# Performance work log

Hardware: AMD Instinct MI355X
Metric: run time of the kernel (lower is better)

## Reference

```python
import jax, jax.numpy as jnp
import numpy as np

N = 100000   # nodes
E = 1600000  # edges
D = 128      # in_dim
H = 128      # hidden_dim
G = 128      # graphs in batch


def setup_inputs() -> dict:
    key = jax.random.key(0)
    ks = jax.random.split(key, 16)
    inp = {
        "x": jax.random.normal(ks[0], (N, D), dtype=jnp.float32),
        "edge_index": jax.random.randint(ks[1], (2, E), 0, N, dtype=jnp.int32),
        "batch": jnp.sort(jax.random.randint(ks[2], (N,), 0, G, dtype=jnp.int32)),
    }
    dims = [(D, H), (H, H), (H, H)]
    k = 3
    for i, (di, dh) in enumerate(dims):
        inp[f"W1_{i}"] = jax.random.normal(ks[k], (di, dh), jnp.float32) * 0.05; k += 1
        inp[f"b1_{i}"] = jnp.zeros((dh,), jnp.float32)
        inp[f"W2_{i}"] = jax.random.normal(ks[k], (dh, dh), jnp.float32) * 0.05; k += 1
        inp[f"b2_{i}"] = jnp.zeros((dh,), jnp.float32)
    return inp


def _gin_layer(x, edge_index, W1, b1, W2, b2):
    # GINConv, eps=0: h_i = MLP(x_i + sum_{j->i} x_j)
    src, dst = edge_index[0], edge_index[1]
    agg = jax.ops.segment_sum(x[src], dst, num_segments=N)  # [N, d]
    h = x + agg
    h = jnp.maximum(h @ W1 + b1, 0.0)  # dropout = identity (eval)
    return h @ W2 + b2


def reference(x, edge_index, batch,
              W1_0, b1_0, W2_0, b2_0,
              W1_1, b1_1, W2_1, b2_1,
              W1_2, b1_2, W2_2, b2_2):
    params = [(W1_0, b1_0, W2_0, b2_0),
              (W1_1, b1_1, W2_1, b2_1),
              (W1_2, b1_2, W2_2, b2_2)]
    h = x
    for (W1, b1, W2, b2) in params:
        h = _gin_layer(h, edge_index, W1, b1, W2, b2)
    # global_mean_pool over batch indices
    sums = jax.ops.segment_sum(h, batch, num_segments=G)             # [G, H]
    cnts = jax.ops.segment_sum(jnp.ones((N,), h.dtype), batch, num_segments=G)
    return sums / jnp.maximum(cnts, 1.0)[:, None]
```

## Files before the change

### kernel.cpp

```cpp
#include <hip/hip_runtime.h>
#include <stdint.h>

#define NN 100000
#define NE 1600000
#define DD 128
#define NG 128
#define NPX 12500
#define NBS 25

using f32x4  = __attribute__((ext_vector_type(4))) float;
using bf16x8 = __attribute__((ext_vector_type(8))) __bf16;

__device__ __forceinline__ unsigned short f2bf(float f) {
  unsigned int u = __builtin_bit_cast(unsigned int, f);
  u = (u + 0x7FFFu + ((u >> 16) & 1u)) >> 16;
  return (unsigned short)u;
}

__device__ __forceinline__ float2 bfu(unsigned int u) {
  float2 r;
  r.x = __builtin_bit_cast(float, u << 16);
  r.y = __builtin_bit_cast(float, u & 0xffff0000u);
  return r;
}

__device__ __forceinline__ void addu4(float* a, uint4 v) {
  float2 p0 = bfu(v.x), p1 = bfu(v.y), p2 = bfu(v.z), p3 = bfu(v.w);
  a[0] += p0.x; a[1] += p0.y; a[2] += p1.x; a[3] += p1.y;
  a[4] += p2.x; a[5] += p2.y; a[6] += p3.x; a[7] += p3.y;
}

union ABu { uint4 q; bf16x8 v; };

__global__ void k_count(const int* __restrict__ dst, int* __restrict__ deg) {
  int xcd = blockIdx.x & 7;
  int e = (blockIdx.x >> 3) * 256 + threadIdx.x;
  if (e >= NE) return;
  int d = dst[e];
  if ((unsigned)(d - xcd * NPX) < (unsigned)NPX) atomicAdd(&deg[d], 1);
}

__global__ __launch_bounds__(1024) void k_scanA(const int* __restrict__ deg,
                                                int* __restrict__ rowptr,
                                                int* __restrict__ bsum) {
  __shared__ int wsum[16];
  const int tid = threadIdx.x, wid = tid >> 6, lane = tid & 63;
  int idx = blockIdx.x * 4096 + tid * 4;
  int v0 = (idx + 0 < NN) ? deg[idx + 0] : 0;
  int v1 = (idx + 1 < NN) ? deg[idx + 1] : 0;
  int v2 = (idx + 2 < NN) ? deg[idx + 2] : 0;
  int v3 = (idx + 3 < NN) ? deg[idx + 3] : 0;
  int tsum = v0 + v1 + v2 + v3;
  int sc = tsum;
  #pragma unroll
  for (int off = 1; off < 64; off <<= 1) {
    int n = __shfl_up(sc, off);
    if (lane >= off) sc += n;
  }
  if (lane == 63) wsum[wid] = sc;
  __syncthreads();
  if (wid == 0 && lane < 16) {
    int w = wsum[lane];
    #pragma unroll
    for (int off = 1; off < 16; off <<= 1) {
      int n = __shfl_up(w, off);
      if (lane >= off) w += n;
    }
    wsum[lane] = w;
  }
  __syncthreads();
  int excl = (wid ? wsum[wid - 1] : 0) + sc - tsum;
  if (idx     <= NN) rowptr[idx]     = excl;
  if (idx + 1 <= NN) rowptr[idx + 1] = excl + v0;
  if (idx + 2 <= NN) rowptr[idx + 2] = excl + v0 + v1;
  if (idx + 3 <= NN) rowptr[idx + 3] = excl + v0 + v1 + v2;
  if (tid == 1023) bsum[blockIdx.x] = wsum[15];
}

__global__ void k_scanB(int* __restrict__ bsum) {
  int lane = threadIdx.x & 63;
  int v = (lane < NBS) ? bsum[lane] : 0;
  int sc = v;
  #pragma unroll
  for (int off = 1; off < 64; off <<= 1) {
    int n = __shfl_up(sc, off);
    if (lane >= off) sc += n;
  }
  if (lane < NBS) bsum[lane] = sc - v;
}

__global__ __launch_bounds__(1024) void k_scanC(int* __restrict__ rowptr,
                                                const int* __restrict__ bsum) {
  int add = bsum[blockIdx.x];
  int idx = blockIdx.x * 4096 + threadIdx.x * 4;
  if (idx     <= NN) rowptr[idx]     += add;
  if (idx + 1 <= NN) rowptr[idx + 1] += add;
  if (idx + 2 <= NN) rowptr[idx + 2] += add;
  if (idx + 3 <= NN) rowptr[idx + 3] += add;
}

__global__ void k_fill(const int* __restrict__ src, const int* __restrict__ dst,
                       const int* __restrict__ rowptr, int* __restrict__ cursor,
                       int* __restrict__ csr) {
  int xcd = blockIdx.x & 7;
  int e = (blockIdx.x >> 3) * 256 + threadIdx.x;
  if (e >= NE) return;
  int d = dst[e];
  if ((unsigned)(d - xcd * NPX) < (unsigned)NPX) {
    int pos = rowptr[d] + atomicAdd(&cursor[d], 1);
    csr[pos] = src[e];
  }
}

__global__ void k_wconv(const float* __restrict__ w0, const float* __restrict__ w1,
                        const float* __restrict__ w2, const float* __restrict__ w3,
                        const float* __restrict__ w4, const float* __restrict__ w5,
                        unsigned short* __restrict__ wt) {
  int idx = blockIdx.x * 256 + threadIdx.x;
  if (idx >= 6 * 16384) return;
  int m = idx >> 14, rem = idx & 16383;
  int n = rem >> 7, k = rem & 127;
  const float* W = (m == 0) ? w0 : (m == 1) ? w1 : (m == 2) ? w2
                 : (m == 3) ? w3 : (m == 4) ? w4 : w5;
  wt[idx] = f2bf(W[k * 128 + n]);
}

__global__ void k_xconv(const float* __restrict__ x, unsigned short* __restrict__ xb) {
  int i = blockIdx.x * 256 + threadIdx.x;
  if (i >= NN * DD / 4) return;
  float4 v = ((const float4*)x)[i];
  uint2 p;
  p.x = (unsigned int)f2bf(v.x) | ((unsigned int)f2bf(v.y) << 16);
  p.y = (unsigned int)f2bf(v.z) | ((unsigned int)f2bf(v.w) << 16);
  ((uint2*)xb)[i] = p;
}

__global__ __launch_bounds__(64) void k_gin(const unsigned short* __restrict__ hb,
                                            const int* __restrict__ rowptr,
                                            const int* __restrict__ csr,
                                            const unsigned short* __restrict__ w1t,
                                            const float* __restrict__ b1,
                                            const unsigned short* __restrict__ w2t,
                                            const float* __restrict__ b2,
                                            unsigned short* __restrict__ hout) {
  __shared__ unsigned short wt_[16 * DD];
  const int lane = threadIdx.x;
  const int r16  = lane & 15;
  const int kg   = lane >> 4;
  const int waveBase = blockIdx.x * 16;
  const uint4* h4 = (const uint4*)hb;

  #pragma unroll
  for (int it = 0; it < 4; ++it) {
    const int lrow = it * 4 + kg;
    const int node = waveBase + lrow;
    float acc[8] = {0.f,0.f,0.f,0.f,0.f,0.f,0.f,0.f};
    if (node < NN) {
      addu4(acc, h4[(size_t)node * 16 + r16]);
      int j = rowptr[node];
      const int je = rowptr[node + 1];
      for (; j + 7 < je; j += 8) {
        int s0 = csr[j],     s1 = csr[j + 1], s2 = csr[j + 2], s3 = csr[j + 3];
        int s4 = csr[j + 4], s5 = csr[j + 5], s6 = csr[j + 6], s7 = csr[j + 7];
        uint4 v0 = h4[(size_t)s0 * 16 + r16];
        uint4 v1 = h4[(size_t)s1 * 16 + r16];
        uint4 v2 = h4[(size_t)s2 * 16 + r16];
        uint4 v3 = h4[(size_t)s3 * 16 + r16];
        uint4 v4 = h4[(size_t)s4 * 16 + r16];
        uint4 v5 = h4[(size_t)s5 * 16 + r16];
        uint4 v6 = h4[(size_t)s6 * 16 + r16];
        uint4 v7 = h4[(size_t)s7 * 16 + r16];
        addu4(acc, v0); addu4(acc, v1); addu4(acc, v2); addu4(acc, v3);
        addu4(acc, v4); addu4(acc, v5); addu4(acc, v6); addu4(acc, v7);
      }
      for (; j + 3 < je; j += 4) {
        int s0 = csr[j], s1 = csr[j + 1], s2 = csr[j + 2], s3 = csr[j + 3];
        uint4 v0 = h4[(size_t)s0 * 16 + r16];
        uint4 v1 = h4[(size_t)s1 * 16 + r16];
        uint4 v2 = h4[(size_t)s2 * 16 + r16];
        uint4 v3 = h4[(size_t)s3 * 16 + r16];
        addu4(acc, v0); addu4(acc, v1); addu4(acc, v2); addu4(acc, v3);
      }
      for (; j < je; ++j) addu4(acc, h4[(size_t)csr[j] * 16 + r16]);
    }
    uint4 p;
    p.x = (unsigned int)f2bf(acc[0]) | ((unsigned int)f2bf(acc[1]) << 16);
    p.y = (unsigned int)f2bf(acc[2]) | ((unsigned int)f2bf(acc[3]) << 16);
    p.z = (unsigned int)f2bf(acc[4]) | ((unsigned int)f2bf(acc[5]) << 16);
    p.w = (unsigned int)f2bf(acc[6]) | ((unsigned int)f2bf(acc[7]) << 16);
    *(uint4*)(wt_ + lrow * DD + ((r16 ^ (lrow & 7)) << 3)) = p;
  }

  f32x4 acc[8];
  #pragma unroll
  for (int nb = 0; nb < 8; ++nb) acc[nb] = (f32x4){0.f, 0.f, 0.f, 0.f};
  #pragma unroll
  for (int s = 0; s < 4; ++s) {
    ABu au;
    au.q = *(const uint4*)(wt_ + r16 * DD + ((((s << 2) + kg) ^ (r16 & 7)) << 3));
    #pragma unroll
    for (int nb = 0; nb < 8; ++nb) {
      ABu bu; bu.q = *(const uint4*)(w1t + (nb * 16 + r16) * DD + s * 32 + kg * 8);
      acc[nb] = __builtin_amdgcn_mfma_f32_16x16x32_bf16(au.v, bu.v, acc[nb], 0, 0, 0);
    }
  }
  #pragma unroll
  for (int nb = 0; nb < 8; ++nb) {
    int n = nb * 16 + r16;
    float bias = b1[n];
    #pragma unroll
    for (int reg = 0; reg < 4; ++reg) {
      int urow = (kg << 2) + reg;
      float v = acc[nb][reg] + bias;
      v = v > 0.f ? v : 0.f;
      wt_[urow * DD + ((((n >> 3) ^ (urow & 7)) << 3) | (n & 7))] = f2bf(v);
    }
  }

  #pragma unroll
  for (int nb = 0; nb < 8; ++nb) acc[nb] = (f32x4){0.f, 0.f, 0.f, 0.f};
  #pragma unroll
  for (int s = 0; s < 4; ++s) {
    ABu au;
    au.q = *(const uint4*)(wt_ + r16 * DD + ((((s << 2) + kg) ^ (r16 & 7)) << 3));
    #pragma unroll
    for (int nb = 0; nb < 8; ++nb) {
      ABu bu; bu.q = *(const uint4*)(w2t + (nb * 16 + r16) * DD + s * 32 + kg * 8);
      acc[nb] = __builtin_amdgcn_mfma_f32_16x16x32_bf16(au.v, bu.v, acc[nb], 0, 0, 0);
    }
  }
  #pragma unroll
  for (int reg = 0; reg < 4; ++reg) {
    int row = waveBase + (kg << 2) + reg;
    if (row < NN) {
      #pragma unroll
      for (int nb = 0; nb < 8; ++nb) {
        int n = nb * 16 + r16;
        hout[row * DD + n] = f2bf(acc[nb][reg] + b2[n]);
      }
    }
  }
}

__global__ __launch_bounds__(256) void k_pool(const unsigned short* __restrict__ hb,
                                              const int* __restrict__ batch,
                                              float* __restrict__ out) {
  const int g  = blockIdx.x;
  const int f2 = threadIdx.x & 63;
  const int rp = threadIdx.x >> 6;
  int lo = 0, hi = NN;
  while (lo < hi) { int m = (lo + hi) >> 1; if (batch[m] < g) lo = m + 1; else hi = m; }
  const int start = lo;
  hi = NN;
  while (lo < hi) { int m = (lo + hi) >> 1; if (batch[m] < g + 1) lo = m + 1; else hi = m; }
  const int end = lo;

  const unsigned int* h32 = (const unsigned int*)hb;
  float2 acc = {0.f, 0.f};
  int i = start + rp;
  for (; i + 4 < end; i += 8) {
    float2 a = bfu(h32[(size_t)i * 64 + f2]);
    float2 b = bfu(h32[(size_t)(i + 4) * 64 + f2]);
    acc.x += a.x + b.x; acc.y += a.y + b.y;
  }
  for (; i < end; i += 4) {
    float2 a = bfu(h32[(size_t)i * 64 + f2]);
    acc.x += a.x; acc.y += a.y;
  }

  __shared__ float2 part[4][64];
  part[rp][f2] = acc;
  __syncthreads();
  if (rp == 0) {
    float2 t0 = part[0][f2], t1 = part[1][f2], t2 = part[2][f2], t3 = part[3][f2];
    float inv = 1.0f / (float)max(end - start, 1);
    out[g * DD + 2 * f2]     = (t0.x + t1.x + t2.x + t3.x) * inv;
    out[g * DD + 2 * f2 + 1] = (t0.y + t1.y + t2.y + t3.y) * inv;
  }
}

extern "C" void kernel_launch(void* const* d_in, const int* in_sizes, int n_in,
                              void* d_out, int out_size, void* d_ws, size_t ws_size,
                              hipStream_t stream) {
  const float* x    = (const float*)d_in[0];
  const int* ei     = (const int*)d_in[1];
  const int* src    = ei;
  const int* dst    = ei + NE;
  const int* batch  = (const int*)d_in[2];

  char* ws = (char*)d_ws;
  size_t off = 0;
  auto alloc = [&](size_t bytes) { char* p = ws + off; off = (off + bytes + 255) & ~(size_t)255; return p; };

  int*  deg    = (int*)alloc(2 * NN * 4);
  int*  cursor = deg + NN;
  int*  rowptr = (int*)alloc((NN + 1) * 4);
  int*  bsum   = (int*)alloc(NBS * 4);
  int*  csr    = (int*)alloc(NE * 4);
  unsigned short* wt = (unsigned short*)alloc(6 * 16384 * 2);
  unsigned short* xb = (unsigned short*)alloc((size_t)NN * DD * 2);
  unsigned short* hA = (unsigned short*)alloc((size_t)NN * DD * 2);
  unsigned short* hB = (unsigned short*)alloc((size_t)NN * DD * 2);

  hipMemsetAsync(deg, 0, 2 * NN * 4, stream);

  k_wconv<<<(6 * 16384 + 255) / 256, 256, 0, stream>>>(
      (const float*)d_in[3], (const float*)d_in[5],
      (const float*)d_in[7], (const float*)d_in[9],
      (const float*)d_in[11], (const float*)d_in[13], wt);
  k_xconv<<<(NN * DD / 4 + 255) / 256, 256, 0, stream>>>(x, xb);

  const int echunks = (NE + 255) / 256;
  k_count<<<8 * echunks, 256, 0, stream>>>(dst, deg);
  k_scanA<<<NBS, 1024, 0, stream>>>(deg, rowptr, bsum);
  k_scanB<<<1, 64, 0, stream>>>(bsum);
  k_scanC<<<NBS, 1024, 0, stream>>>(rowptr, bsum);
  k_fill<<<8 * echunks, 256, 0, stream>>>(src, dst, rowptr, cursor, csr);

  const unsigned short* hin = xb;
  unsigned short* houts[3] = {hA, hB, hA};
  for (int l = 0; l < 3; ++l) {
    k_gin<<<(NN + 15) / 16, 64, 0, stream>>>(
        hin, rowptr, csr,
        wt + (2 * l) * 16384, (const float*)d_in[4 + 4 * l],
        wt + (2 * l + 1) * 16384, (const float*)d_in[6 + 4 * l], houts[l]);
    hin = houts[l];
  }

  k_pool<<<NG, 256, 0, stream>>>(hin, batch, (float*)d_out);
}
```

Baseline: 612.5 us.

## Split GIN block work across four waves for gather and MLP

Each 16-node block now runs on four waves instead of one. Each wave gathers neighbour sums for 4 nodes, and in the two MLP GEMMs each wave computes 2 of the 8 output column tiles. Barriers are added between the gather, the first GEMM, the ReLU writeback to shared memory, and the second GEMM. The aim is more memory-level parallelism in the latency-bound gather and less serial work per wave, at the cost of block-wide synchronisation and more threads per block.

Result: faster. 589.0 us (-3.8%).

```diff
diff --git a/kernel.cpp b/kernel.cpp
--- a/kernel.cpp
+++ b/kernel.cpp
@@ -135,25 +135,25 @@
   ((uint2*)xb)[i] = p;
 }
 
-__global__ __launch_bounds__(64) void k_gin(const unsigned short* __restrict__ hb,
-                                            const int* __restrict__ rowptr,
-                                            const int* __restrict__ csr,
-                                            const unsigned short* __restrict__ w1t,
-                                            const float* __restrict__ b1,
-                                            const unsigned short* __restrict__ w2t,
-                                            const float* __restrict__ b2,
-                                            unsigned short* __restrict__ hout) {
+__global__ __launch_bounds__(256) void k_gin(const unsigned short* __restrict__ hb,
+                                             const int* __restrict__ rowptr,
+                                             const int* __restrict__ csr,
+                                             const unsigned short* __restrict__ w1t,
+                                             const float* __restrict__ b1,
+                                             const unsigned short* __restrict__ w2t,
+                                             const float* __restrict__ b2,
+                                             unsigned short* __restrict__ hout) {
   __shared__ unsigned short wt_[16 * DD];
-  const int lane = threadIdx.x;
+  const int wv   = threadIdx.x >> 6;
+  const int lane = threadIdx.x & 63;
   const int r16  = lane & 15;
   const int kg   = lane >> 4;
-  const int waveBase = blockIdx.x * 16;
+  const int blockBase = blockIdx.x * 16;
   const uint4* h4 = (const uint4*)hb;
 
-  #pragma unroll
-  for (int it = 0; it < 4; ++it) {
-    const int lrow = it * 4 + kg;
-    const int node = waveBase + lrow;
+  {
+    const int lrow = wv * 4 + kg;
+    const int node = blockBase + lrow;
     float acc[8] = {0.f,0.f,0.f,0.f,0.f,0.f,0.f,0.f};
     if (node < NN) {
       addu4(acc, h4[(size_t)node * 16 + r16]);
@@ -190,53 +190,59 @@
     p.w = (unsigned int)f2bf(acc[6]) | ((unsigned int)f2bf(acc[7]) << 16);
     *(uint4*)(wt_ + lrow * DD + ((r16 ^ (lrow & 7)) << 3)) = p;
   }
-
-  f32x4 acc[8];
-  #pragma unroll
-  for (int nb = 0; nb < 8; ++nb) acc[nb] = (f32x4){0.f, 0.f, 0.f, 0.f};
+  __syncthreads();
+
+  f32x4 acc[2];
+  acc[0] = (f32x4){0.f, 0.f, 0.f, 0.f};
+  acc[1] = (f32x4){0.f, 0.f, 0.f, 0.f};
   #pragma unroll
   for (int s = 0; s < 4; ++s) {
     ABu au;
     au.q = *(const uint4*)(wt_ + r16 * DD + ((((s << 2) + kg) ^ (r16 & 7)) << 3));
     #pragma unroll
-    for (int nb = 0; nb < 8; ++nb) {
+    for (int q = 0; q < 2; ++q) {
+      int nb = wv * 2 + q;
       ABu bu; bu.q = *(const uint4*)(w1t + (nb * 16 + r16) * DD + s * 32 + kg * 8);
-      acc[nb] = __builtin_amdgcn_mfma_f32_16x16x32_bf16(au.v, bu.v, acc[nb], 0, 0, 0);
-    }
-  }
-  #pragma unroll
-  for (int nb = 0; nb < 8; ++nb) {
+      acc[q] = __builtin_amdgcn_mfma_f32_16x16x32_bf16(au.v, bu.v, acc[q], 0, 0, 0);
+    }
+  }
+  __syncthreads();
+  #pragma unroll
+  for (int q = 0; q < 2; ++q) {
+    int nb = wv * 2 + q;
     int n = nb * 16 + r16;
     float bias = b1[n];
     #pragma unroll
     for (int reg = 0; reg < 4; ++reg) {
       int urow = (kg << 2) + reg;
-      float v = acc[nb][reg] + bias;
+      float v = acc[q][reg] + bias;
       v = v > 0.f ? v : 0.f;
       wt_[urow * DD + ((((n >> 3) ^ (urow & 7)) << 3) | (n & 7))] = f2bf(v);
     }
   }
-
-  #pragma unroll
-  for (int nb = 0; nb < 8; ++nb) acc[nb] = (f32x4){0.f, 0.f, 0.f, 0.f};
+  __syncthreads();
+
+  acc[0] = (f32x4){0.f, 0.f, 0.f, 0.f};
+  acc[1] = (f32x4){0.f, 0.f, 0.f, 0.f};
   #pragma unroll
   for (int s = 0; s < 4; ++s) {
     ABu au;
     au.q = *(const uint4*)(wt_ + r16 * DD + ((((s << 2) + kg) ^ (r16 & 7)) << 3));
     #pragma unroll
-    for (int nb = 0; nb < 8; ++nb) {
+    for (int q = 0; q < 2; ++q) {
+      int nb = wv * 2 + q;
       ABu bu; bu.q = *(const uint4*)(w2t + (nb * 16 + r16) * DD + s * 32 + kg * 8);
-      acc[nb] = __builtin_amdgcn_mfma_f32_16x16x32_bf16(au.v, bu.v, acc[nb], 0, 0, 0);
+      acc[q] = __builtin_amdgcn_mfma_f32_16x16x32_bf16(au.v, bu.v, acc[q], 0, 0, 0);
     }
   }
   #pragma unroll
   for (int reg = 0; reg < 4; ++reg) {
-    int row = waveBase + (kg << 2) + reg;
+    int row = blockBase + (kg << 2) + reg;
     if (row < NN) {
       #pragma unroll
-      for (int nb = 0; nb < 8; ++nb) {
-        int n = nb * 16 + r16;
-        hout[row * DD + n] = f2bf(acc[nb][reg] + b2[n]);
+      for (int q = 0; q < 2; ++q) {
+        int n = (wv * 2 + q) * 16 + r16;
+        hout[row * DD + n] = f2bf(acc[q][reg] + b2[n]);
       }
     }
   }
@@ -320,7 +326,7 @@
   const unsigned short* hin = xb;
   unsigned short* houts[3] = {hA, hB, hA};
   for (int l = 0; l < 3; ++l) {
-    k_gin<<<(NN + 15) / 16, 64, 0, stream>>>(
+    k_gin<<<(NN + 15) / 16, 256, 0, stream>>>(
         hin, rowptr, csr,
         wt + (2 * l) * 16384, (const float*)d_in[4 + 4 * l],
         wt + (2 * l + 1) * 16384, (const float*)d_in[6 + 4 * l], houts[l]);
```
